# Optimization experiments

Measured on AMD Instinct MI355X. Metric: run time of the kernel, lower is better.

The kernel has to match this reference:

```python
import jax, jax.numpy as jnp
import numpy as np

N_EMBD = 768
N_HEAD = 12
LN_EPS = 1e-5

def _ln(x, g, b):
    mu = jnp.mean(x, axis=-1, keepdims=True)
    var = jnp.mean(jnp.square(x - mu), axis=-1, keepdims=True)
    return (x - mu) * jax.lax.rsqrt(var + LN_EPS) * g + b

def setup_inputs() -> dict:
    key = jax.random.key(0)
    ks = jax.random.split(key, 16)
    C = N_EMBD
    s = lambda n: 0.02
    return {
        "x": jax.random.normal(ks[0], (4, 2048, C), jnp.float32),
        "ln1_g": jnp.ones((C,), jnp.float32),
        "ln1_b": jnp.zeros((C,), jnp.float32),
        "w_attn": jax.random.normal(ks[1], (C, 3 * C), jnp.float32) * s(C),
        "b_attn": jnp.zeros((3 * C,), jnp.float32),
        "w_proj": jax.random.normal(ks[2], (C, C), jnp.float32) * s(C),
        "b_proj": jnp.zeros((C,), jnp.float32),
        "ln2_g": jnp.ones((C,), jnp.float32),
        "ln2_b": jnp.zeros((C,), jnp.float32),
        "w_fc": jax.random.normal(ks[3], (C, 4 * C), jnp.float32) * s(C),
        "b_fc": jnp.zeros((4 * C,), jnp.float32),
        "w_fc2": jax.random.normal(ks[4], (4 * C, C), jnp.float32) * s(C),
        "b_fc2": jnp.zeros((C,), jnp.float32),
    }

def reference(x, ln1_g, ln1_b, w_attn, b_attn, w_proj, b_proj,
              ln2_g, ln2_b, w_fc, b_fc, w_fc2, b_fc2):
    B, T, C = x.shape
    H = N_HEAD
    hd = C // H
    # --- attention sublayer (pre-LN) ---
    h = _ln(x, ln1_g, ln1_b)
    qkv = h @ w_attn + b_attn                       # [B,T,3C]
    q, k, v = jnp.split(qkv, 3, axis=-1)
    q = q.reshape(B, T, H, hd).transpose(0, 2, 1, 3)  # [B,H,T,hd]
    k = k.reshape(B, T, H, hd).transpose(0, 2, 1, 3)
    v = v.reshape(B, T, H, hd).transpose(0, 2, 1, 3)
    aw = jnp.einsum("bhqd,bhkd->bhqk", q, k) / jnp.sqrt(jnp.float32(hd))
    mask = jnp.tril(jnp.ones((T, T), bool))
    aw = jnp.where(mask, aw, -jnp.inf)
    aw = jax.nn.softmax(aw, axis=-1)
    cv = jnp.einsum("bhqk,bhkd->bhqd", aw, v)       # [B,H,T,hd]
    cv = cv.transpose(0, 2, 1, 3).reshape(B, T, C)
    x = cv @ w_proj + b_proj + x
    # --- MLP sublayer (pre-LN) ---
    h = _ln(x, ln2_g, ln2_b)
    h = jax.nn.gelu(h @ w_fc + b_fc, approximate=True)
    x = h @ w_fc2 + b_fc2 + x
    return x
```

## Files before the change

### kernel.cpp

```cpp
#include <hip/hip_runtime.h>
#include <hip/hip_bf16.h>

typedef __attribute__((ext_vector_type(8))) short short8;
typedef __attribute__((ext_vector_type(4))) float f32x4;
typedef __attribute__((ext_vector_type(16))) float f32x16;
typedef __attribute__((ext_vector_type(4))) unsigned int u32x4;

__device__ __forceinline__ short bf16_bits(float f) {
    __hip_bfloat16 h = __float2bfloat16(f);
    return __builtin_bit_cast(short, h);
}

#define GLOAD_LDS16(g, l) __builtin_amdgcn_global_load_lds( \
    (const __attribute__((address_space(1))) void*)(g),     \
    (__attribute__((address_space(3))) void*)(l), 16, 0, 0)

__device__ __forceinline__ f32x16 mfma32(short8 a, short8 b, f32x16 c) {
    return __builtin_amdgcn_mfma_f32_32x32x16_bf16(a, b, c, 0, 0, 0);
}

__device__ __forceinline__ void half_swap(unsigned a, unsigned b,
                                          unsigned& x, unsigned& y) {
#if __has_builtin(__builtin_amdgcn_permlane32_swap)
    typedef __attribute__((ext_vector_type(2))) unsigned int uint2v;
    uint2v r = __builtin_amdgcn_permlane32_swap(a, b, false, false);
    x = r[0]; y = r[1];
#else
    unsigned bx_ = __shfl_xor((int)b, 32);
    unsigned ax_ = __shfl_xor((int)a, 32);
    int hi = (threadIdx.x & 63) >> 5;
    x = hi ? bx_ : a;
    y = hi ? b : ax_;
#endif
}

__global__ __launch_bounds__(256) void wcast_t(const float* __restrict__ w,
                                               short* __restrict__ wt, int K, int N) {
    __shared__ float tile[32][33];
    int n0 = blockIdx.x * 32, k0 = blockIdx.y * 32;
    int tx = threadIdx.x, ty = threadIdx.y;
#pragma unroll
    for (int i = 0; i < 32; i += 8)
        tile[ty + i][tx] = w[(size_t)(k0 + ty + i) * N + n0 + tx];
    __syncthreads();
#pragma unroll
    for (int i = 0; i < 32; i += 8)
        wt[(size_t)(n0 + ty + i) * K + k0 + tx] = bf16_bits(tile[tx][ty + i]);
}

__global__ __launch_bounds__(256) void ln_kernel(const float* __restrict__ x,
                                                 const float* __restrict__ g,
                                                 const float* __restrict__ bta,
                                                 short* __restrict__ out) {
    int row = blockIdx.x;
    const float* xr = x + (size_t)row * 768;
    int t = threadIdx.x;
    float v0 = xr[t], v1 = xr[t + 256], v2 = xr[t + 512];
    float s = v0 + v1 + v2;
#pragma unroll
    for (int o = 32; o; o >>= 1) s += __shfl_xor(s, o);
    __shared__ float red[8];
    int wid = t >> 6, lane = t & 63;
    if (lane == 0) red[wid] = s;
    __syncthreads();
    s = red[0] + red[1] + red[2] + red[3];
    float mu = s * (1.0f / 768.0f);
    float d0 = v0 - mu, d1 = v1 - mu, d2 = v2 - mu;
    float q = d0 * d0 + d1 * d1 + d2 * d2;
#pragma unroll
    for (int o = 32; o; o >>= 1) q += __shfl_xor(q, o);
    if (lane == 0) red[4 + wid] = q;
    __syncthreads();
    q = red[4] + red[5] + red[6] + red[7];
    float rstd = rsqrtf(q * (1.0f / 768.0f) + 1e-5f);
    short* orow = out + (size_t)row * 768;
    orow[t]       = bf16_bits(d0 * rstd * g[t]       + bta[t]);
    orow[t + 256] = bf16_bits(d1 * rstd * g[t + 256] + bta[t + 256]);
    orow[t + 512] = bf16_bits(d2 * rstd * g[t + 512] + bta[t + 512]);
}

#define BM 128
#define BN 128
#define BK 64

template <int EPI>
__global__ __launch_bounds__(256) void gemm_bt(const short* __restrict__ A,
                                               const short* __restrict__ BT,
                                               const float* __restrict__ bias,
                                               const float* __restrict__ res,
                                               void* __restrict__ outp,
                                               int M, int N, int K) {
    __shared__ short smem[2 * BM * BK];
    const int tid = threadIdx.x;
    const int lane = tid & 63;
    const int wid = tid >> 6;
    const int wr = wid >> 1, wc = wid & 1;
    const int laneb = lane & 15, laneh = lane >> 4;
    const int rowB0 = blockIdx.y * BM;
    const int colB0 = blockIdx.x * BN;

    f32x4 acc[4][4] = {};

    const char* gA = (const char*)(A + (size_t)rowB0 * K);
    const char* gB = (const char*)(BT + (size_t)colB0 * K);
    char* ldsA = (char*)smem;
    char* ldsB = (char*)(smem + BM * BK);
    const int wbase = tid & ~63;

    for (int k0 = 0; k0 < K; k0 += BK) {
        __syncthreads();
#pragma unroll
        for (int sub = 0; sub < 4; ++sub) {
            int idx = sub * 256 + tid;
            int row = idx >> 3;
            int inner = (idx & 7) << 4;
            int src = inner ^ ((row & 7) << 4);
            size_t gofs = (size_t)row * (K * 2) + (size_t)k0 * 2 + src;
            int lbase = (sub * 256 + wbase) * 16;
            GLOAD_LDS16(gA + gofs, ldsA + lbase);
            GLOAD_LDS16(gB + gofs, ldsB + lbase);
        }
        __syncthreads();
#pragma unroll
        for (int kk = 0; kk < 2; ++kk) {
            short8 af[4], bf[4];
#pragma unroll
            for (int m = 0; m < 4; ++m) {
                int r = wr * 64 + m * 16 + laneb;
                int kb = (kk * 64 + (laneh << 4)) ^ ((r & 7) << 4);
                af[m] = *(const short8*)(ldsA + r * 128 + kb);
            }
#pragma unroll
            for (int n = 0; n < 4; ++n) {
                int r = wc * 64 + n * 16 + laneb;
                int kb = (kk * 64 + (laneh << 4)) ^ ((r & 7) << 4);
                bf[n] = *(const short8*)(ldsB + r * 128 + kb);
            }
#pragma unroll
            for (int m = 0; m < 4; ++m)
#pragma unroll
                for (int n = 0; n < 4; ++n)
                    acc[m][n] = __builtin_amdgcn_mfma_f32_16x16x32_bf16(af[m], bf[n],
                                                                        acc[m][n], 0, 0, 0);
        }
    }

    const int r0 = rowB0 + wr * 64;
    const int c0 = colB0 + wc * 64;
#pragma unroll
    for (int m = 0; m < 4; ++m) {
#pragma unroll
        for (int n = 0; n < 4; ++n) {
            int col = c0 + n * 16 + laneb;
            float bv = bias[col];
#pragma unroll
            for (int j = 0; j < 4; ++j) {
                int row = r0 + m * 16 + (laneh << 2) + j;
                float v = acc[m][n][j] + bv;
                size_t o = (size_t)row * N + col;
                if constexpr (EPI == 1) {
                    ((float*)outp)[o] = v + res[o];
                } else if constexpr (EPI == 2) {
                    float u = 0.7978845608028654f * (v + 0.044715f * v * v * v);
                    ((short*)outp)[o] = bf16_bits(0.5f * v * (1.0f + tanhf(u)));
                } else {
                    ((short*)outp)[o] = bf16_bits(v);
                }
            }
        }
    }
}

__global__ __launch_bounds__(256) void build_vt(const short* __restrict__ qkv,
                                                short* __restrict__ vT) {
    constexpr int T = 2048, H = 12, LDQ = 2304;
    __shared__ short tile[32][33];
    int bh = blockIdx.z;
    int b = bh / H, h = bh % H;
    int t0 = blockIdx.x * 32, d0 = blockIdx.y * 32;
    int tx = threadIdx.x, ty = threadIdx.y;
    const short* src = qkv + (size_t)(b * T) * LDQ + 1536 + h * 64;
#pragma unroll
    for (int i = 0; i < 32; i += 8)
        tile[ty + i][tx] = src[(size_t)(t0 + ty + i) * LDQ + d0 + tx];
    __syncthreads();
    short* dst = vT + (size_t)bh * 64 * T;
#pragma unroll
    for (int i = 0; i < 32; i += 8)
        dst[(size_t)(d0 + ty + i) * T + t0 + tx] = tile[tx][ty + i];
}

__global__ __launch_bounds__(256) void attn_kernel(const short* __restrict__ qkv,
                                                   const short* __restrict__ vT,
                                                   short* __restrict__ cv) {
    constexpr int T = 2048, C = 768, H = 12, LDQ = 2304;
    constexpr int OST = 36;
    constexpr float SCL = 0.125f * 1.44269504088896f;
    __shared__ float ldsO[4 * 32 * OST];
    __shared__ float ldsM[128], ldsL[128];
    const int tid = threadIdx.x;
    const int lane = tid & 63;
    const int w = tid >> 6;
    const int l31 = lane & 31;
    const int hi = lane >> 5;

    const int g = blockIdx.x;
    const int xcd = g & 7;
    const int t = g >> 3;
    const int bh = xcd * 6 + (t >> 5);
    const int j = t & 31;
    const int b = bh / H, h = bh % H;

    const short* qbase = qkv + (size_t)(b * T) * LDQ + h * 64;
    const short* kbase = qbase + C;
    const short* vtb = vT + (size_t)bh * 64 * T;

#pragma unroll 1
    for (int pi = 0; pi < 2; ++pi) {
        const int c = pi ? 63 - j : j;
        const int q0 = c * 32;

        short8 qf[4];
        {
            const short* p = qbase + (size_t)(q0 + l31) * LDQ + hi * 8;
            qf[0] = *(const short8*)(p);
            qf[1] = *(const short8*)(p + 16);
            qf[2] = *(const short8*)(p + 32);
            qf[3] = *(const short8*)(p + 48);
        }

        f32x16 o0 = {}, o1 = {};
        float m = -3e38f, lsum = 0.f;

        for (int kt = w; kt <= c; kt += 4) {
            const int k0 = kt * 32;
            const short* kp = kbase + (size_t)(k0 + l31) * LDQ + hi * 8;
            short8 kf0 = *(const short8*)(kp);
            short8 kf1 = *(const short8*)(kp + 16);
            short8 kf2 = *(const short8*)(kp + 32);
            short8 kf3 = *(const short8*)(kp + 48);

            f32x16 s = {};
            s = mfma32(kf0, qf[0], s);
            s = mfma32(kf1, qf[1], s);
            s = mfma32(kf2, qf[2], s);
            s = mfma32(kf3, qf[3], s);

            const bool diag = (kt == c);
            float pmax = -3e38f;
#pragma unroll
            for (int r = 0; r < 16; ++r) {
                float v = s[r] * SCL;
                if (diag) {
                    int key = (r & 3) + 8 * (r >> 2) + 4 * hi;
                    if (key > l31) v = -3e38f;
                }
                s[r] = v;
                pmax = fmaxf(pmax, v);
            }
            pmax = fmaxf(pmax, __shfl_xor(pmax, 32));

            if (__any(pmax > m + 11.5f)) {
                float mn = fmaxf(m, pmax);
                float corr = exp2f(m - mn);
                lsum *= corr;
                m = mn;
#pragma unroll
                for (int r = 0; r < 16; ++r) {
                    float cr = __shfl(corr, (r & 3) + 8 * (r >> 2) + 4 * hi);
                    o0[r] *= cr;
                    o1[r] *= cr;
                }
            }

            float rs = 0.f;
#pragma unroll
            for (int r = 0; r < 16; ++r) {
                float p = exp2f(s[r] - m);
                s[r] = p;
                rs += p;
            }
            rs += __shfl_xor(rs, 32);
            lsum += rs;

            unsigned pk[8];
#pragma unroll
            for (int i = 0; i < 8; ++i)
                pk[i] = ((unsigned)(unsigned short)bf16_bits(s[2 * i + 1]) << 16) |
                        (unsigned short)bf16_bits(s[2 * i]);
            unsigned a0, a2, a1, a3, b0, b2, b1, b3;
            half_swap(pk[0], pk[2], a0, a2);
            half_swap(pk[1], pk[3], a1, a3);
            half_swap(pk[4], pk[6], b0, b2);
            half_swap(pk[5], pk[7], b1, b3);
            u32x4 w0v = {a0, a1, a2, a3};
            u32x4 w1v = {b0, b1, b2, b3};
            short8 pa0 = __builtin_bit_cast(short8, w0v);
            short8 pa1 = __builtin_bit_cast(short8, w1v);

            const short* vp0 = vtb + (size_t)l31 * T + k0 + hi * 8;
            const short* vp1 = vp0 + (size_t)32 * T;
            short8 v00 = *(const short8*)(vp0);
            short8 v01 = *(const short8*)(vp0 + 16);
            short8 v10 = *(const short8*)(vp1);
            short8 v11 = *(const short8*)(vp1 + 16);

            o0 = mfma32(pa0, v00, o0);
            o0 = mfma32(pa1, v01, o0);
            o1 = mfma32(pa0, v10, o1);
            o1 = mfma32(pa1, v11, o1);
        }

        float* myO = ldsO + w * 32 * OST;
#pragma unroll
        for (int r = 0; r < 16; ++r) {
            int q = (r & 3) + 8 * (r >> 2) + 4 * hi;
            myO[q * OST + l31] = o0[r];
        }
        if (hi == 0) {
            ldsM[w * 32 + l31] = m;
            ldsL[w * 32 + l31] = lsum;
        }
        __syncthreads();

        const int q = w * 8 + (lane >> 3);
        const int dj = (lane & 7) * 4;
        float mw[4], M, inv;
        {
#pragma unroll
            for (int u = 0; u < 4; ++u) mw[u] = ldsM[u * 32 + q];
            M = fmaxf(fmaxf(mw[0], mw[1]), fmaxf(mw[2], mw[3]));
            float L = 0.f;
            f32x4 s0 = {};
#pragma unroll
            for (int u = 0; u < 4; ++u) {
                float sc = exp2f(mw[u] - M);
                mw[u] = sc;
                L += ldsL[u * 32 + q] * sc;
                f32x4 a = *(const f32x4*)(ldsO + (u * 32 + q) * OST + dj);
#pragma unroll
                for (int jj = 0; jj < 4; ++jj) s0[jj] += a[jj] * sc;
            }
            inv = 1.0f / L;
            short* dst = cv + (size_t)(b * T + q0 + q) * C + h * 64 + dj;
#pragma unroll
            for (int jj = 0; jj < 4; ++jj) dst[jj] = bf16_bits(s0[jj] * inv);
        }
        __syncthreads();

#pragma unroll
        for (int r = 0; r < 16; ++r) {
            int qq = (r & 3) + 8 * (r >> 2) + 4 * hi;
            myO[qq * OST + l31] = o1[r];
        }
        __syncthreads();

        {
            f32x4 s1 = {};
#pragma unroll
            for (int u = 0; u < 4; ++u) {
                float sc = mw[u];
                f32x4 a = *(const f32x4*)(ldsO + (u * 32 + q) * OST + dj);
#pragma unroll
                for (int jj = 0; jj < 4; ++jj) s1[jj] += a[jj] * sc;
            }
            short* dst = cv + (size_t)(b * T + q0 + q) * C + h * 64 + 32 + dj;
#pragma unroll
            for (int jj = 0; jj < 4; ++jj) dst[jj] = bf16_bits(s1[jj] * inv);
        }
        __syncthreads();
    }
}

extern "C" void kernel_launch(void* const* d_in, const int* in_sizes, int n_in,
                              void* d_out, int out_size, void* d_ws, size_t ws_size,
                              hipStream_t stream) {
    const float* x      = (const float*)d_in[0];
    const float* ln1_g  = (const float*)d_in[1];
    const float* ln1_b  = (const float*)d_in[2];
    const float* w_attn = (const float*)d_in[3];
    const float* b_attn = (const float*)d_in[4];
    const float* w_proj = (const float*)d_in[5];
    const float* b_proj = (const float*)d_in[6];
    const float* ln2_g  = (const float*)d_in[7];
    const float* ln2_b  = (const float*)d_in[8];
    const float* w_fc   = (const float*)d_in[9];
    const float* b_fc   = (const float*)d_in[10];
    const float* w_fc2  = (const float*)d_in[11];
    const float* b_fc2  = (const float*)d_in[12];

    char* ws = (char*)d_ws;
    short* wT_attn = (short*)(ws + 0);
    short* wT_proj = (short*)(ws + 3538944);
    short* wT_fc   = (short*)(ws + 4718592);
    short* wT_fc2  = (short*)(ws + 9437184);
    short* bufA    = (short*)(ws + 14155776);
    short* qkvb    = (short*)(ws + 26738688);
    short* vT      = (short*)(ws + 64487424);
    float* x1      = (float*)(ws + 77070336);

    dim3 blkT(32, 8);
    wcast_t<<<dim3(72, 24), blkT, 0, stream>>>(w_attn, wT_attn, 768, 2304);
    wcast_t<<<dim3(24, 24), blkT, 0, stream>>>(w_proj, wT_proj, 768, 768);
    wcast_t<<<dim3(96, 24), blkT, 0, stream>>>(w_fc, wT_fc, 768, 3072);
    wcast_t<<<dim3(24, 96), blkT, 0, stream>>>(w_fc2, wT_fc2, 3072, 768);

    ln_kernel<<<8192, 256, 0, stream>>>(x, ln1_g, ln1_b, bufA);
    gemm_bt<0><<<dim3(18, 64), 256, 0, stream>>>(bufA, wT_attn, b_attn, nullptr,
                                                 qkvb, 8192, 2304, 768);
    build_vt<<<dim3(64, 2, 48), blkT, 0, stream>>>(qkvb, vT);
    attn_kernel<<<dim3(1536), 256, 0, stream>>>(qkvb, vT, bufA);
    gemm_bt<1><<<dim3(6, 64), 256, 0, stream>>>(bufA, wT_proj, b_proj, x,
                                                x1, 8192, 768, 768);
    ln_kernel<<<8192, 256, 0, stream>>>(x1, ln2_g, ln2_b, bufA);
    gemm_bt<2><<<dim3(24, 64), 256, 0, stream>>>(bufA, wT_fc, b_fc, nullptr,
                                                 qkvb, 8192, 3072, 768);
    gemm_bt<1><<<dim3(6, 64), 256, 0, stream>>>(qkvb, wT_fc2, b_fc2, x1,
                                                d_out, 8192, 768, 3072);
}
```

Before: 345.8 us.

## Fold softmax scale into Q weights, swizzle GEMM tiles, bound attention occupancy

Pre-multiplies the Q columns of the QKV weight and bias by the softmax scale (times log2 e) during the bf16 cast, so the attention inner loop no longer multiplies every score. Remaps GEMM workgroup indices with an XCD-aware swizzle so that tiles sharing rows land on the same XCD, aiming for better L2 reuse. Adds a minimum-occupancy hint of 6 to the attention kernel's launch bounds, which may limit registers and cause spills. Scaling Q after bf16 rounding changes numerics slightly.

Measured after the change: 396.4 us. 14.6% more time.

```diff
diff --git a/kernel.cpp b/kernel.cpp
--- a/kernel.cpp
+++ b/kernel.cpp
@@ -35,7 +35,8 @@
 }
 
 __global__ __launch_bounds__(256) void wcast_t(const float* __restrict__ w,
-                                               short* __restrict__ wt, int K, int N) {
+                                               short* __restrict__ wt, int K, int N,
+                                               int qcols, float qscale) {
     __shared__ float tile[32][33];
     int n0 = blockIdx.x * 32, k0 = blockIdx.y * 32;
     int tx = threadIdx.x, ty = threadIdx.y;
@@ -44,8 +45,19 @@
         tile[ty + i][tx] = w[(size_t)(k0 + ty + i) * N + n0 + tx];
     __syncthreads();
 #pragma unroll
-    for (int i = 0; i < 32; i += 8)
-        wt[(size_t)(n0 + ty + i) * K + k0 + tx] = bf16_bits(tile[tx][ty + i]);
+    for (int i = 0; i < 32; i += 8) {
+        int n = n0 + ty + i;
+        float v = tile[tx][ty + i];
+        if (n < qcols) v *= qscale;
+        wt[(size_t)n * K + k0 + tx] = bf16_bits(v);
+    }
+}
+
+__global__ __launch_bounds__(256) void scale_bias(const float* __restrict__ b,
+                                                  float* __restrict__ out,
+                                                  int n, int qcols, float s) {
+    int i = blockIdx.x * 256 + threadIdx.x;
+    if (i < n) out[i] = (i < qcols) ? b[i] * s : b[i];
 }
 
 __global__ __launch_bounds__(256) void ln_kernel(const float* __restrict__ x,
@@ -96,8 +108,13 @@
     const int wid = tid >> 6;
     const int wr = wid >> 1, wc = wid & 1;
     const int laneb = lane & 15, laneh = lane >> 4;
-    const int rowB0 = blockIdx.y * BM;
-    const int colB0 = blockIdx.x * BN;
+
+    const int nwg = (int)(gridDim.x * gridDim.y);
+    const int g0 = (int)(blockIdx.y * gridDim.x + blockIdx.x);
+    int swz = g0;
+    if (!(nwg & 7)) swz = (g0 & 7) * (nwg >> 3) + (g0 >> 3);
+    const int rowB0 = (swz / (int)gridDim.x) * BM;
+    const int colB0 = (swz % (int)gridDim.x) * BN;
 
     f32x4 acc[4][4] = {};
 
@@ -190,12 +207,11 @@
         dst[(size_t)(d0 + ty + i) * T + t0 + tx] = tile[tx][ty + i];
 }
 
-__global__ __launch_bounds__(256) void attn_kernel(const short* __restrict__ qkv,
-                                                   const short* __restrict__ vT,
-                                                   short* __restrict__ cv) {
+__global__ __launch_bounds__(256, 6) void attn_kernel(const short* __restrict__ qkv,
+                                                      const short* __restrict__ vT,
+                                                      short* __restrict__ cv) {
     constexpr int T = 2048, C = 768, H = 12, LDQ = 2304;
     constexpr int OST = 36;
-    constexpr float SCL = 0.125f * 1.44269504088896f;
     __shared__ float ldsO[4 * 32 * OST];
     __shared__ float ldsM[128], ldsL[128];
     const int tid = threadIdx.x;
@@ -250,7 +266,7 @@
             float pmax = -3e38f;
 #pragma unroll
             for (int r = 0; r < 16; ++r) {
-                float v = s[r] * SCL;
+                float v = s[r];
                 if (diag) {
                     int key = (r & 3) + 8 * (r >> 2) + 4 * hi;
                     if (key > l31) v = -3e38f;
@@ -389,6 +405,8 @@
     const float* w_fc2  = (const float*)d_in[11];
     const float* b_fc2  = (const float*)d_in[12];
 
+    const float SCL = 0.125f * 1.44269504088896f;
+
     char* ws = (char*)d_ws;
     short* wT_attn = (short*)(ws + 0);
     short* wT_proj = (short*)(ws + 3538944);
@@ -398,15 +416,17 @@
     short* qkvb    = (short*)(ws + 26738688);
     short* vT      = (short*)(ws + 64487424);
     float* x1      = (float*)(ws + 77070336);
+    float* b_attn_s = (float*)(ws + 102236160);
 
     dim3 blkT(32, 8);
-    wcast_t<<<dim3(72, 24), blkT, 0, stream>>>(w_attn, wT_attn, 768, 2304);
-    wcast_t<<<dim3(24, 24), blkT, 0, stream>>>(w_proj, wT_proj, 768, 768);
-    wcast_t<<<dim3(96, 24), blkT, 0, stream>>>(w_fc, wT_fc, 768, 3072);
-    wcast_t<<<dim3(24, 96), blkT, 0, stream>>>(w_fc2, wT_fc2, 3072, 768);
+    wcast_t<<<dim3(72, 24), blkT, 0, stream>>>(w_attn, wT_attn, 768, 2304, 768, SCL);
+    wcast_t<<<dim3(24, 24), blkT, 0, stream>>>(w_proj, wT_proj, 768, 768, 0, 1.0f);
+    wcast_t<<<dim3(96, 24), blkT, 0, stream>>>(w_fc, wT_fc, 768, 3072, 0, 1.0f);
+    wcast_t<<<dim3(24, 96), blkT, 0, stream>>>(w_fc2, wT_fc2, 3072, 768, 0, 1.0f);
+    scale_bias<<<9, 256, 0, stream>>>(b_attn, b_attn_s, 2304, 768, SCL);
 
     ln_kernel<<<8192, 256, 0, stream>>>(x, ln1_g, ln1_b, bufA);
-    gemm_bt<0><<<dim3(18, 64), 256, 0, stream>>>(bufA, wT_attn, b_attn, nullptr,
+    gemm_bt<0><<<dim3(18, 64), 256, 0, stream>>>(bufA, wT_attn, b_attn_s, nullptr,
                                                  qkvb, 8192, 2304, 768);
     build_vt<<<dim3(64, 2, 48), blkT, 0, stream>>>(qkvb, vT);
     attn_kernel<<<dim3(1536), 256, 0, stream>>>(qkvb, vT, bufA);
```
